# Kernel optimization log

Measured on AMD Instinct MI355X. Metric: run time of the kernel, lower is better.

## Reference

```python
import jax, jax.numpy as jnp
import numpy as np

# Module init config (from init_kwargs): output_size=(96,192,192), method='nearest'
OUT_D, OUT_H, OUT_W = 96, 192, 192


def _nearest_idx(out_size, in_size):
    # TF2 tf.image.resize(method='nearest') uses half-pixel centers:
    # src = floor((dst + 0.5) * in/out), clipped to valid range.
    scale = in_size / out_size
    idx = jnp.floor((jnp.arange(out_size, dtype=jnp.float32) + 0.5) * scale)
    return jnp.clip(idx.astype(jnp.int32), 0, in_size - 1)


def reference(image):
    # image: (b, d, h, w, c)
    # Original module: pass 1 resizes each depth slice (h,w)->(h_out,w_out);
    # pass 2 resizes each height slice (d,w)->(d_out,w_out). The second w-resize
    # is identity (w already w_out), so nearest resize factorizes per-axis.
    b, d, h, w, c = image.shape
    x = jnp.take(image, _nearest_idx(OUT_H, h), axis=2)  # (b,d,H,w,c)
    x = jnp.take(x, _nearest_idx(OUT_W, w), axis=3)      # (b,d,H,W,c)
    x = jnp.take(x, _nearest_idx(OUT_D, d), axis=1)      # (b,D,H,W,c)
    return x


def setup_inputs() -> dict:
    key = jax.random.key(0)
    image = jax.random.normal(key, (2, 64, 128, 128, 16), dtype=jnp.float32)
    return {"image": image}
```

## Files before the change

### kernel.cpp

```cpp
#include <hip/hip_runtime.h>


typedef float f4 __attribute__((ext_vector_type(4)));

#define OUT_D 96u
#define OUT_H 192u
#define OUT_W 192u
#define IN_D 64u
#define IN_H 128u
#define IN_W 128u

#define TOTAL4 (2u * OUT_D * OUT_H * OUT_W * 4u)

__global__ __launch_bounds__(256) void Resize3D_52304111731438_kernel(
    const f4* __restrict__ in, f4* __restrict__ out) {
    unsigned base = blockIdx.x * 1024u + threadIdx.x;

    f4 v[4];
#pragma unroll
    for (int k = 0; k < 4; ++k) {
        unsigned i  = base + (unsigned)k * 256u;
        unsigned c4 = i & 3u;
        unsigned t  = i >> 2;
        unsigned w  = t % OUT_W;  t /= OUT_W;
        unsigned h  = t % OUT_H;  t /= OUT_H;
        unsigned d  = t % OUT_D;
        unsigned b  = t / OUT_D;

        unsigned sw = (2u * w + 1u) / 3u;
        unsigned sh = (2u * h + 1u) / 3u;
        unsigned sd = (2u * d + 1u) / 3u;

        unsigned src = (((b * IN_D + sd) * IN_H + sh) * IN_W + sw) * 4u + c4;
        v[k] = in[src];
    }

#pragma unroll
    for (int k = 0; k < 4; ++k) {
        __builtin_nontemporal_store(v[k], &out[base + (unsigned)k * 256u]);
    }
}

extern "C" void kernel_launch(void* const* d_in, const int* in_sizes, int n_in,
                              void* d_out, int out_size, void* d_ws, size_t ws_size,
                              hipStream_t stream) {
    const f4* in = (const f4*)d_in[0];
    f4* out = (f4*)d_out;
    const unsigned blocks = TOTAL4 / 1024u;
    Resize3D_52304111731438_kernel<<<blocks, 256, 0, stream>>>(in, out);
}
```

Baseline: 517.4 us.

## Map each block to four output rows and swizzle blocks across XCDs

Each block now handles four full output rows (192 width by 16 channels) of one depth slice. The per-element div/mod index math is replaced by per-block row math plus per-thread column offsets computed once. Block IDs are remapped so that consecutive logical blocks run on the same XCD, which is meant to improve L2 reuse of duplicated source rows and depth slices. Each thread now does 12 loads and stores instead of 4, with fewer blocks launched.

```diff
diff --git a/kernel.cpp b/kernel.cpp
--- a/kernel.cpp
+++ b/kernel.cpp
@@ -10,34 +10,53 @@
 #define IN_H 128u
 #define IN_W 128u
 
-#define TOTAL4 (2u * OUT_D * OUT_H * OUT_W * 4u)
+#define N_BLOCKS 9216u
+#define BLOCKS_PER_XCD (N_BLOCKS / 8u)
 
 __global__ __launch_bounds__(256) void Resize3D_52304111731438_kernel(
     const f4* __restrict__ in, f4* __restrict__ out) {
-    unsigned base = blockIdx.x * 1024u + threadIdx.x;
+    unsigned bid = blockIdx.x;
+    bid = (bid & 7u) * BLOCKS_PER_XCD + (bid >> 3);
 
-    f4 v[4];
+    const unsigned tid = threadIdx.x;
+
+    unsigned q  = bid % 48u;
+    unsigned bd = bid / 48u;
+    unsigned d  = bd % 96u;
+    unsigned b  = bd / 96u;
+    unsigned h0 = q * 4u;
+    unsigned sd = (2u * d + 1u) / 3u;
+
+    unsigned off[3];
 #pragma unroll
-    for (int k = 0; k < 4; ++k) {
-        unsigned i  = base + (unsigned)k * 256u;
-        unsigned c4 = i & 3u;
-        unsigned t  = i >> 2;
-        unsigned w  = t % OUT_W;  t /= OUT_W;
-        unsigned h  = t % OUT_H;  t /= OUT_H;
-        unsigned d  = t % OUT_D;
-        unsigned b  = t / OUT_D;
+    for (int k = 0; k < 3; ++k) {
+        unsigned r  = tid + (unsigned)k * 256u;
+        unsigned w  = r >> 2;
+        unsigned c4 = r & 3u;
+        unsigned sw = (2u * w + 1u) / 3u;
+        off[k] = sw * 4u + c4;
+    }
 
-        unsigned sw = (2u * w + 1u) / 3u;
+    const f4* __restrict__ slice = in + (size_t)(b * IN_D + sd) * (IN_H * IN_W * 4u);
+    f4* __restrict__ oblk = out + (size_t)bid * 3072u + tid;
+
+    f4 v[4][3];
+#pragma unroll
+    for (int row = 0; row < 4; ++row) {
+        unsigned h  = h0 + (unsigned)row;
         unsigned sh = (2u * h + 1u) / 3u;
-        unsigned sd = (2u * d + 1u) / 3u;
-
-        unsigned src = (((b * IN_D + sd) * IN_H + sh) * IN_W + sw) * 4u + c4;
-        v[k] = in[src];
+        const f4* __restrict__ irow = slice + sh * (IN_W * 4u);
+#pragma unroll
+        for (int k = 0; k < 3; ++k) v[row][k] = irow[off[k]];
     }
 
 #pragma unroll
-    for (int k = 0; k < 4; ++k) {
-        __builtin_nontemporal_store(v[k], &out[base + (unsigned)k * 256u]);
+    for (int row = 0; row < 4; ++row) {
+#pragma unroll
+        for (int k = 0; k < 3; ++k) {
+            __builtin_nontemporal_store(v[row][k],
+                                        &oblk[(unsigned)row * 768u + (unsigned)k * 256u]);
+        }
     }
 }
 
@@ -46,6 +65,5 @@
                               hipStream_t stream) {
     const f4* in = (const f4*)d_in[0];
     f4* out = (f4*)d_out;
-    const unsigned blocks = TOTAL4 / 1024u;
-    Resize3D_52304111731438_kernel<<<blocks, 256, 0, stream>>>(in, out);
+    Resize3D_52304111731438_kernel<<<N_BLOCKS, 256, 0, stream>>>(in, out);
 }
```

Measured after the change: 535.7 us. 1.04x slower.
